# Optimization experiments

Hardware: AMD Instinct MI355X
Metric: run time of the kernel (lower is better)

The kernel has to match this reference:

```python
import jax, jax.numpy as jnp
import numpy as np

B, T, F_, S, H = 4096, 128, 96, 128, 512
IMPUTE_WEIGHT = 0.3
L1, L2 = 0.01, 0.1


def setup_inputs() -> dict:
    key = jax.random.key(0)
    ks = jax.random.split(key, 28)
    def n(k, shape, s=0.05):
        return jax.random.normal(k, shape, jnp.float32) * s
    return dict(
        values=jax.random.normal(ks[0], (B, T, F_), jnp.float32),
        masks=jax.random.bernoulli(ks[1], 0.8, (B, T, F_)).astype(jnp.float32),
        deltas=jax.random.uniform(ks[2], (B, T, F_), jnp.float32, 0.0, 5.0),
        statics=jax.random.normal(ks[3], (B, S), jnp.float32),
        static_masks=jax.random.bernoulli(ks[4], 0.8, (B, S)).astype(jnp.float32),
        labels=jax.random.bernoulli(ks[5], 0.5, (B,)).astype(jnp.float32),
        fr_W=n(ks[6], (S, S)), fr_b=n(ks[7], (S,)),
        d1_W=n(ks[8], (H, S)), d1_b=n(ks[9], (H,)),
        d2_W=n(ks[10], (H, H)), d2_b=n(ks[11], (H,)),
        d3_W=n(ks[12], (H, H)), d3_b=n(ks[13], (H,)),
        td_W=n(ks[14], (H, F_)), td_b=n(ks[15], (H,)),
        hist_W=n(ks[16], (F_, H)), hist_b=n(ks[17], (F_,)),
        st_W=n(ks[18], (F_, S)), st_b=n(ks[19], (F_,)),
        real_W=n(ks[20], (F_, F_)), real_b=n(ks[21], (F_,)),
        lstm_Wih=n(ks[22], (4 * H, 2 * F_)), lstm_Whh=n(ks[23], (4 * H, H)),
        lstm_bih=n(ks[24], (4 * H,)), lstm_bhh=n(ks[25], (4 * H,)),
        out_W=n(ks[26], (1, H)), out_b=n(ks[27], (1,)),
    )


def reference(values, masks, deltas, statics, static_masks, labels,
              fr_W, fr_b, d1_W, d1_b, d2_W, d2_b, d3_W, d3_b,
              td_W, td_b, hist_W, hist_b, st_W, st_b, real_W, real_b,
              lstm_Wih, lstm_Whh, lstm_bih, lstm_bhh, out_W, out_b):
    sg = jax.lax.stop_gradient
    # ---- MultiModal (dropout = identity in inference) ----
    s_h = statics @ fr_W.T + fr_b
    s_c = static_masks * statics + (1.0 - static_masks) * s_h
    s_tc = s_c
    s_loss = jnp.sum(jnp.abs(statics - s_c) * static_masks) / (jnp.sum(static_masks) + 1e-5)
    s_loss = s_loss + IMPUTE_WEIGHT * L2 * jnp.sum(jnp.abs(jnp.diagonal(sg(fr_W))))
    h = jax.nn.relu(s_c @ d1_W.T + d1_b)
    h = jax.nn.relu(h @ d2_W.T + d2_b)
    h = jax.nn.relu(h @ d3_W.T + d3_b)                 # initial hidden state
    c = jnp.zeros((values.shape[0], H), values.dtype)
    st_term = s_tc @ st_W.T + st_b

    def step(carry, xs):
        h, c, xl = carry
        x, m, d = xs                                   # each [B, F_]
        gamma = jnp.exp(-jax.nn.relu(d @ td_W.T + td_b))
        h = h * gamma
        x_c = (x @ real_W.T + real_b) + (h @ hist_W.T + hist_b) + st_term
        xl = xl + jnp.sum(jnp.abs(x - x_c) * m) / (jnp.sum(m) + 1e-5)
        c_c = m * x + (1.0 - m) * x_c
        inp = jnp.concatenate([c_c, m], axis=1)        # [B, 2*F_]
        gates = inp @ lstm_Wih.T + lstm_bih + h @ lstm_Whh.T + lstm_bhh
        i, f, g, o = jnp.split(gates, 4, axis=1)       # torch LSTMCell gate order
        c = jax.nn.sigmoid(f) * c + jax.nn.sigmoid(i) * jnp.tanh(g)
        h = jax.nn.sigmoid(o) * jnp.tanh(c)
        return (h, c, xl), c_c

    xs = (jnp.swapaxes(values, 0, 1), jnp.swapaxes(masks, 0, 1), jnp.swapaxes(deltas, 0, 1))
    (h, c, x_loss), imps = jax.lax.scan(step, (h, c, jnp.float32(0.0)), xs)
    imputations = jnp.swapaxes(imps, 0, 1)             # [B, T, F_]

    y_h = h @ out_W.T + out_b                          # [B, 1]
    z = y_h[:, 0]
    # BCE with logits, mean reduction (stable form)
    y_loss = jnp.mean(jnp.maximum(z, 0.0) - z * labels + jnp.log1p(jnp.exp(-jnp.abs(z))))
    # regularizers on .data (stop-gradient in torch semantics)
    r_loss = L1 * (jnp.sum(jnp.abs(sg(real_W))) + jnp.sum(jnp.abs(sg(hist_W))) + jnp.sum(jnp.abs(sg(st_W))))
    r_loss = r_loss + L2 * jnp.sum(jnp.abs(jnp.diagonal(sg(real_W))))
    loss = y_loss + r_loss + IMPUTE_WEIGHT * x_loss + s_loss
    return (loss, jax.nn.sigmoid(y_h), imputations)
```

## Files before the change

### kernel.cpp

```cpp
#include <hip/hip_runtime.h>
#include <math.h>

#define Bn 4096
#define Tn 128
#define Fn 96
#define Sn 128
#define Hn 512

typedef __attribute__((ext_vector_type(8))) short bf16x8;
typedef __attribute__((ext_vector_type(4))) float f32x4;

#define GC(p) ((const __attribute__((address_space(1))) void*)(p))
#define LC(p) ((__attribute__((address_space(3))) void*)(p))

__device__ __forceinline__ short tobf(float f){
  unsigned u = __float_as_uint(f);
  unsigned r = (u + 0x7fffu + ((u>>16)&1u)) >> 16;
  return (short)r;
}
__device__ __forceinline__ float bf2f(short s){
  return __uint_as_float(((unsigned)(unsigned short)s)<<16);
}
__device__ __forceinline__ float sigmf_(float x){ return 1.0f/(1.0f+expf(-x)); }

__device__ __forceinline__ int haddr(int row, int k){
  int c = k & 63;
  return ((k>>6)<<10) + (row<<6) + ((((c>>3) ^ (row&7)))<<3) + (c&7);
}

__device__ __forceinline__ void stage_tile(const short* gsrc, size_t sstride, int k0,
                                           short* lt, int rows, int wid, int lane, int nw){
  int calls = rows >> 3;
  for (int c = wid; c < calls; c += nw){
    int r = (c<<3) + (lane>>3);
    int ch = (lane&7) ^ (r&7);
    const short* gp = gsrc + (size_t)r*sstride + k0 + (ch<<3);
    __builtin_amdgcn_global_load_lds(GC(gp), LC(lt + (c<<9)), 16, 0, 0);
  }
}
__device__ __forceinline__ bf16x8 frag(const short* lt, int row, int ch){
  return *(const bf16x8*)(lt + (row<<6) + ((ch ^ (row&7))<<3));
}


__global__ void k_pack_td(const float* __restrict__ tdW, short* __restrict__ tdWp){
  int i = blockIdx.x*256 + threadIdx.x;
  if (i >= 512*128) return;
  int n = i>>7, k = i&127;
  tdWp[i] = (k < Fn) ? tobf(tdW[n*Fn + k]) : (short)0;
}
__global__ void k_pack_x(const float* __restrict__ realW, const float* __restrict__ histW,
                         const float* __restrict__ realb, const float* __restrict__ histb,
                         short* __restrict__ Wxp, float* __restrict__ bxp){
  int i = blockIdx.x*256 + threadIdx.x;
  if (i < Fn) bxp[i] = realb[i] + histb[i];
  if (i >= Fn*640) return;
  int f = i/640, k = i - f*640;
  float v = 0.f;
  if (k < 512) v = histW[f*Hn + k];
  else if (k < 608) v = realW[f*Fn + (k-512)];
  Wxp[i] = tobf(v);
}
__global__ void k_pack_g(const float* __restrict__ Wih, const float* __restrict__ Whh,
                         const float* __restrict__ bih, const float* __restrict__ bhh,
                         short* __restrict__ Wgp, float* __restrict__ bgp){
  int i = blockIdx.x*256 + threadIdx.x;
  if (i >= 16*128*704) return;
  int k = i % 704; int nc = i / 704;
  int pb = nc >> 7, ncol = nc & 127;
  int jj = pb*32 + (ncol >> 2), g = ncol & 3;
  int n = g*Hn + jj;
  float v;
  if (k < 512) v = Whh[(size_t)n*Hn + k];
  else if (k < 608) v = Wih[(size_t)n*192 + (k-512)];
  else v = Wih[(size_t)n*192 + 96 + (k-608)];
  Wgp[i] = tobf(v);
  if (k == 0) bgp[nc] = bih[n] + bhh[n];
}
__global__ void k_cvt(const float* __restrict__ src, short* __restrict__ dst, int n){
  int i = blockIdx.x*256 + threadIdx.x;
  if (i < n) dst[i] = tobf(src[i]);
}


__global__ void k_static(const float* __restrict__ statics, const float* __restrict__ smask,
                         const float* __restrict__ frW, const float* __restrict__ frb,
                         float* __restrict__ s_c){
  __shared__ float row[Sn];
  int b = blockIdx.x, j = threadIdx.x;
  row[j] = statics[b*Sn + j];
  __syncthreads();
  float acc = frb[j];
  #pragma unroll 4
  for (int k = 0; k < Sn; k++) acc += row[k] * frW[j*Sn + k];
  float m = smask[b*Sn + j];
  s_c[b*Sn + j] = m * row[j] + (1.0f - m) * acc;
}

template<int K, bool RELU, bool WF32>
__global__ __launch_bounds__(512) void k_gemm(const short* __restrict__ A,
    const short* __restrict__ B, const float* __restrict__ bias,
    short* __restrict__ outb, float* __restrict__ outf){
  __shared__ __align__(16) short stA[2][8192], stB[2][8192];
  const int tid = threadIdx.x, lane = tid&63, wid = tid>>6;
  const int mb = blockIdx.x >> 2, nb = blockIdx.x & 3;
  const int r0 = mb*128, c0 = nb*128;
  const int wM = wid>>1, wN = wid&1, lr = lane&15, lq = lane>>4;
  f32x4 acc[2][4];
  #pragma unroll
  for (int m=0;m<2;m++)
    #pragma unroll
    for (int n=0;n<4;n++) acc[m][n] = (f32x4){0,0,0,0};
  constexpr int NS = K/64;
  stage_tile(A + (size_t)r0*K, K, 0, stA[0], 128, wid, lane, 8);
  stage_tile(B + (size_t)c0*K, K, 0, stB[0], 128, wid, lane, 8);
  __syncthreads();
  for (int kc=0; kc<NS; kc++){
    if (kc < NS-1){
      stage_tile(A + (size_t)r0*K, K, (kc+1)*64, stA[(kc+1)&1], 128, wid, lane, 8);
      stage_tile(B + (size_t)c0*K, K, (kc+1)*64, stB[(kc+1)&1], 128, wid, lane, 8);
    }
    #pragma unroll
    for (int kk=0;kk<2;kk++){
      int ch = (kk<<2) + lq;
      bf16x8 af[2];
      #pragma unroll
      for (int m=0;m<2;m++) af[m] = frag(stA[kc&1], wM*32 + m*16 + lr, ch);
      #pragma unroll
      for (int n=0;n<4;n++){
        bf16x8 bf = frag(stB[kc&1], wN*64 + n*16 + lr, ch);
        #pragma unroll
        for (int m=0;m<2;m++)
          acc[m][n] = __builtin_amdgcn_mfma_f32_16x16x32_bf16(af[m], bf, acc[m][n],0,0,0);
      }
    }
    __syncthreads();
  }
  #pragma unroll
  for (int m=0;m<2;m++)
    #pragma unroll
    for (int n=0;n<4;n++){
      int col = c0 + wN*64 + n*16 + lr;
      float bv = bias[col];
      #pragma unroll
      for (int reg=0;reg<4;reg++){
        int row = r0 + wM*32 + m*16 + (lq<<2) + reg;
        float v = acc[m][n][reg] + bv;
        if (RELU) v = fmaxf(v, 0.f);
        outb[(size_t)row*512 + col] = tobf(v);
        if (WF32) outf[(size_t)row*512 + col] = v;
      }
    }
}

template<int K, int N, bool RELU>
__global__ void k_mlp(const float* __restrict__ in, const float* __restrict__ W,
                      const float* __restrict__ bias, float* __restrict__ out){
  __shared__ float row[K];
  int b = blockIdx.x;
  for (int i = threadIdx.x; i < K; i += blockDim.x) row[i] = in[b*K + i];
  __syncthreads();
  for (int n = threadIdx.x; n < N; n += blockDim.x){
    float acc = bias[n];
    #pragma unroll 4
    for (int k = 0; k < K; k++) acc += row[k] * W[n*K + k];
    if (RELU) acc = fmaxf(acc, 0.0f);
    out[b*N + n] = acc;
  }
}

__global__ __launch_bounds__(512) void k_dxc(int t,
    const float* __restrict__ values, const float* __restrict__ masks,
    const float* __restrict__ deltas,
    const short* __restrict__ tdWp, const float* __restrict__ tdb,
    const short* __restrict__ Wxp,  const float* __restrict__ bxp,
    const float* __restrict__ st,   const float* __restrict__ h_g,
    short* __restrict__ inp, float* __restrict__ out_imp,
    float* __restrict__ num, float* __restrict__ den){
  __shared__ __align__(16) short Adel[2*1024];
  __shared__ __align__(16) short A2[10*1024];
  __shared__ short sm[16*96];
  __shared__ __align__(16) short Bbig[65536];
  __shared__ float wred[8], wred2[8];
  const int tid = threadIdx.x, lane = tid&63, wid = tid>>6;
  const int r0 = blockIdx.x*16;
  const int lr = lane&15, lq = lane>>4;

  float4 xv4, mv4, dv4;
  const bool act = tid < 384;
  int ar=0, af0=0;
  if (act){
    ar = tid/24; int fq = tid - ar*24; af0 = fq*4;
    size_t gb = ((size_t)(r0+ar)*Tn + t)*Fn + af0;
    xv4 = *(const float4*)(values + gb);
    mv4 = *(const float4*)(masks  + gb);
    dv4 = *(const float4*)(deltas + gb);
  }

  float hreg[16];
  #pragma unroll
  for (int nq=0;nq<4;nq++){
    int col = nq*128 + wid*16 + lr;
    #pragma unroll
    for (int reg=0;reg<4;reg++)
      hreg[nq*4+reg] = h_g[(size_t)(r0 + (lq<<2) + reg)*Hn + col];
  }
  float streg[4] = {0.f,0.f,0.f,0.f};
  if (wid < 6){
    int f = wid*16 + lr;
    #pragma unroll
    for (int reg=0;reg<4;reg++)
      streg[reg] = st[(size_t)(r0 + (lq<<2) + reg)*Fn + f];
  }

  #pragma unroll
  for (int s=0; s<8; s++){
    int nq = s>>1, kc = s&1;
    stage_tile(tdWp + (size_t)(nq*128)*128, 128, kc*64, Bbig + s*8192, 128, wid, lane, 8);
  }

  if (act){
    #pragma unroll
    for (int j=0;j<4;j++){
      int f = af0 + j;
      float xv = ((const float*)&xv4)[j];
      float mv = ((const float*)&mv4)[j];
      float dv = ((const float*)&dv4)[j];
      sm[ar*96 + f] = tobf(mv);
      inp[(size_t)(r0+ar)*704 + 608 + f] = tobf(mv);
      A2 [haddr(ar, 512+f)] = tobf(xv);
      Adel[haddr(ar, f)]    = tobf(dv);
    }
  }
  { int r = tid>>5, cz = tid&31;
    Adel[haddr(r,  96+cz)] = 0;
    A2  [haddr(r, 608+cz)] = 0;
  }
  __syncthreads();

  f32x4 accd[4];
  #pragma unroll
  for (int q=0;q<4;q++) accd[q] = (f32x4){0,0,0,0};
  #pragma unroll
  for (int s=0; s<8; s++){
    int nq = s>>1, kc = s&1;
    #pragma unroll
    for (int kk=0;kk<2;kk++){
      int ch = (kk<<2) + lq;
      bf16x8 afr = frag(Adel + kc*1024, lr, ch);
      bf16x8 bfr = frag(Bbig + s*8192, wid*16 + lr, ch);
      accd[nq] = __builtin_amdgcn_mfma_f32_16x16x32_bf16(afr, bfr, accd[nq], 0,0,0);
    }
  }
  __syncthreads();

  #pragma unroll
  for (int kx=0; kx<10; kx++)
    stage_tile(Wxp, 640, kx*64, Bbig + kx*6144, 96, wid, lane, 8);

  #pragma unroll
  for (int nq=0;nq<4;nq++){
    int col = nq*128 + wid*16 + lr;
    float tb = tdb[col];
    #pragma unroll
    for (int reg=0;reg<4;reg++){
      int row = (lq<<2) + reg;
      float v = accd[nq][reg] + tb;
      float hd = hreg[nq*4+reg] * __expf(-fmaxf(v,0.f));
      A2[haddr(row, col)] = tobf(hd);
      inp[(size_t)(r0+row)*704 + col] = tobf(hd);
    }
  }
  __syncthreads();

  f32x4 accx = (f32x4){0,0,0,0};
  if (wid < 6){
    #pragma unroll
    for (int kx=0; kx<10; kx++)
      #pragma unroll
      for (int kk=0;kk<2;kk++){
        int ch = (kk<<2) + lq;
        bf16x8 afr = frag(A2 + kx*1024, lr, ch);
        bf16x8 bfr = frag(Bbig + kx*6144, wid*16 + lr, ch);
        accx = __builtin_amdgcn_mfma_f32_16x16x32_bf16(afr, bfr, accx, 0,0,0);
      }
  }
  float lsum = 0.f, msum = 0.f;
  if (wid < 6){
    int f = wid*16 + lr;
    float bx = bxp[f];
    #pragma unroll
    for (int reg=0;reg<4;reg++){
      int row = (lq<<2) + reg;
      float xcv = accx[reg] + bx + streg[reg];
      float xv = bf2f(A2[haddr(row, 512+f)]);
      float mv = bf2f(sm[row*96 + f]);
      lsum += fabsf(xv - xcv)*mv;
      msum += mv;
      float cc = mv*xv + (1.f-mv)*xcv;
      inp[(size_t)(r0+row)*704 + 512 + f] = tobf(cc);
      out_imp[((size_t)(r0+row)*Tn + t)*Fn + f] = cc;
    }
  }
  #pragma unroll
  for (int o=32;o>0;o>>=1){ lsum += __shfl_down(lsum, o); msum += __shfl_down(msum, o); }
  if (lane==0){ wred[wid] = lsum; wred2[wid] = msum; }
  __syncthreads();
  if (tid==0){
    float s2 = 0.f, s3 = 0.f;
    #pragma unroll
    for (int w2=0;w2<8;w2++){ s2 += wred[w2]; s3 += wred2[w2]; }
    atomicAdd(&num[t], s2);
    atomicAdd(&den[t], s3);
  }
}

__global__ __launch_bounds__(512, 4) void k_gates(int t, const short* __restrict__ inp,
    const short* __restrict__ Wgp, const float* __restrict__ bgp,
    float* __restrict__ h_g, float* __restrict__ c_g){
  __shared__ __align__(16) short stA[2][8192], stB[2][8192];
  const int tid = threadIdx.x, lane = tid&63, wid = tid>>6;
  const int mb = blockIdx.x & 31, pb = blockIdx.x >> 5;
  const int r0 = mb*128;
  const short* gA = inp + (size_t)r0*704;
  const short* gB = Wgp + (size_t)pb*128*704;
  const int wM = wid>>1, wN = wid&1, lr = lane&15, lq = lane>>4;
  f32x4 acc[2][4];
  #pragma unroll
  for (int m=0;m<2;m++)
    #pragma unroll
    for (int n=0;n<4;n++) acc[m][n] = (f32x4){0,0,0,0};

  stage_tile(gA, 704, 0, stA[0], 128, wid, lane, 8);
  stage_tile(gB, 704, 0, stB[0], 128, wid, lane, 8);
  __syncthreads();

  for (int kc=0; kc<11; kc++){
    if (kc < 10){
      stage_tile(gA, 704, (kc+1)*64, stA[(kc+1)&1], 128, wid, lane, 8);
      stage_tile(gB, 704, (kc+1)*64, stB[(kc+1)&1], 128, wid, lane, 8);
    }
    #pragma unroll
    for (int kk=0;kk<2;kk++){
      int ch = (kk<<2) + lq;
      bf16x8 af[2];
      #pragma unroll
      for (int m=0;m<2;m++) af[m] = frag(stA[kc&1], wM*32 + m*16 + lr, ch);
      #pragma unroll
      for (int n=0;n<4;n++){
        bf16x8 bf = frag(stB[kc&1], wN*64 + n*16 + lr, ch);
        #pragma unroll
        for (int m=0;m<2;m++)
          acc[m][n] = __builtin_amdgcn_mfma_f32_16x16x32_bf16(af[m], bf, acc[m][n],0,0,0);
      }
    }
    __syncthreads();
  }

  const int g = lane&3;
  const float s_  = (g==2) ? 2.0f : -1.0f;
  const float ca_ = (g==2) ? -2.0f : 1.0f;
  const float cb_ = (g==2) ? 1.0f : 0.0f;
  #pragma unroll
  for (int m=0;m<2;m++){
    int row = r0 + wM*32 + m*16 + (lq<<2) + g;
    #pragma unroll
    for (int n=0;n<4;n++){
      int colbase = wN*64 + n*16 + lr;
      float b = bgp[pb*128 + colbase];
      float q0 = 1.f/(1.f+__expf(s_*(acc[m][n][0]+b))); float a0 = q0*ca_+cb_;
      float q1 = 1.f/(1.f+__expf(s_*(acc[m][n][1]+b))); float a1 = q1*ca_+cb_;
      float q2 = 1.f/(1.f+__expf(s_*(acc[m][n][2]+b))); float a2 = q2*ca_+cb_;
      float q3 = 1.f/(1.f+__expf(s_*(acc[m][n][3]+b))); float a3 = q3*ca_+cb_;
      int i1=g^1, i2=g^2, i3=g^3;
      float p1 = (i1==0)?a0:(i1==1)?a1:(i1==2)?a2:a3;
      float p2 = (i2==0)?a0:(i2==1)?a1:(i2==2)?a2:a3;
      float p3 = (i3==0)?a0:(i3==1)?a1:(i3==2)?a2:a3;
      float ow = (g==0)?a0:(g==1)?a1:(g==2)?a2:a3;
      float t1 = __shfl_xor(p1, 1, 64);
      float t2 = __shfl_xor(p2, 2, 64);
      float t3 = __shfl_xor(p3, 3, 64);
      float si = (g==0)?ow:(g==1)?t1:(g==2)?t2:t3;
      float sf = (g==1)?ow:(g==0)?t1:(g==3)?t2:t3;
      float tg = (g==2)?ow:(g==3)?t1:(g==0)?t2:t3;
      float so = (g==3)?ow:(g==2)?t1:(g==1)?t2:t3;
      int jh = pb*32 + (colbase>>2);
      size_t idx = (size_t)row*Hn + jh;
      float co = c_g[idx];
      float cn = sf*co + si*tg;
      float targ = fminf(fmaxf(2.0f*cn,-60.f),60.f);
      float e = __expf(targ); float th = (e-1.f)/(e+1.f);
      c_g[idx] = cn;
      h_g[idx] = so*th;
    }
  }
}


__global__ void k_out(const float* __restrict__ h_g, const float* __restrict__ outW,
                      const float* __restrict__ outb, const float* __restrict__ labels,
                      float* __restrict__ out_sig, float* __restrict__ yacc){
  int b = blockIdx.x, lane = threadIdx.x;
  float s = 0.f;
  for (int k = lane; k < Hn; k += 64) s += h_g[(size_t)b*Hn + k] * outW[k];
  #pragma unroll
  for (int o = 32; o > 0; o >>= 1) s += __shfl_down(s, o);
  if (lane == 0){
    float z = s + outb[0];
    out_sig[b] = sigmf_(z);
    float yl = fmaxf(z, 0.f) - z*labels[b] + log1pf(expf(-fabsf(z)));
    atomicAdd(yacc, yl);
  }
}

__global__ void k_loss(const float* __restrict__ realW, const float* __restrict__ histW,
                       const float* __restrict__ stW,   const float* __restrict__ frW,
                       const float* __restrict__ num,   const float* __restrict__ den,
                       const float* __restrict__ yacc,  float* __restrict__ out0){
  int tid = threadIdx.x;
  float r1 = 0.f;
  for (int i = tid; i < Fn*Fn; i += 256) r1 += fabsf(realW[i]);
  for (int i = tid; i < Fn*Hn; i += 256) r1 += fabsf(histW[i]);
  for (int i = tid; i < Fn*Sn; i += 256) r1 += fabsf(stW[i]);
  float rd = 0.f;
  for (int i = tid; i < Fn; i += 256) rd += fabsf(realW[i*Fn + i]);
  float fd = 0.f;
  for (int i = tid; i < Sn; i += 256) fd += fabsf(frW[i*Sn + i]);
  float xl = 0.f;
  for (int t = tid; t < Tn; t += 256) xl += num[t] / (den[t] + 1e-5f);
  float v = 0.01f*r1 + 0.1f*rd + 0.3f*xl + 0.03f*fd;
  __shared__ float red[256];
  red[tid] = v; __syncthreads();
  for (int o = 128; o > 0; o >>= 1){ if (tid < o) red[tid] += red[tid + o]; __syncthreads(); }
  if (tid == 0) out0[0] = red[0] + yacc[0] / (float)Bn;
}


extern "C" void kernel_launch(void* const* d_in, const int* in_sizes, int n_in,
                              void* d_out, int out_size, void* d_ws, size_t ws_size,
                              hipStream_t stream){
  const float* values = (const float*)d_in[0];
  const float* masks  = (const float*)d_in[1];
  const float* deltas = (const float*)d_in[2];
  const float* statics= (const float*)d_in[3];
  const float* smask  = (const float*)d_in[4];
  const float* labels = (const float*)d_in[5];
  const float* frW = (const float*)d_in[6];
  const float* frb = (const float*)d_in[7];
  const float* d1W = (const float*)d_in[8];
  const float* d1b = (const float*)d_in[9];
  const float* d2W = (const float*)d_in[10];
  const float* d2b = (const float*)d_in[11];
  const float* d3W = (const float*)d_in[12];
  const float* d3b = (const float*)d_in[13];
  const float* tdW = (const float*)d_in[14];
  const float* tdb = (const float*)d_in[15];
  const float* histW = (const float*)d_in[16];
  const float* histb = (const float*)d_in[17];
  const float* stW = (const float*)d_in[18];
  const float* stb = (const float*)d_in[19];
  const float* realW = (const float*)d_in[20];
  const float* realb = (const float*)d_in[21];
  const float* Wih = (const float*)d_in[22];
  const float* Whh = (const float*)d_in[23];
  const float* bih = (const float*)d_in[24];
  const float* bhh = (const float*)d_in[25];
  const float* outW = (const float*)d_in[26];
  const float* outb = (const float*)d_in[27];

  float* out0    = (float*)d_out;
  float* out_sig = out0 + 1;
  float* out_imp = out0 + 1 + Bn;

  float* wsf  = (float*)d_ws;
  float* s_c  = wsf;  wsf += Bn*Sn;
  float* h    = wsf;  wsf += (size_t)Bn*Hn;
  float* c    = wsf;  wsf += (size_t)Bn*Hn;
  float* st   = wsf;  wsf += Bn*Fn;
  float* den  = wsf;  wsf += Tn;
  float* num  = wsf;  wsf += Tn;
  float* yacc = num + Tn;
  wsf += 1;
  float* bxp  = wsf;  wsf += 128;
  float* bgp  = wsf;  wsf += 2048;
  size_t off = ((size_t)(wsf - (float*)d_ws) + 3u) & ~(size_t)3u;
  short* wss  = (short*)((float*)d_ws + off);
  short* tdWp = wss;  wss += 512*128;
  short* Wxp  = wss;  wss += 96*640;
  short* Wgp  = wss;  wss += (size_t)16*128*704;
  short* inp  = wss;  wss += (size_t)Bn*704;
  short* wd1  = wss;  wss += 512*128;
  short* wd2  = wss;  wss += 512*512;
  short* wd3  = wss;  wss += 512*512;
  short* act0 = wss;  wss += (size_t)Bn*128;
  short* actA = wss;  wss += (size_t)Bn*512;
  short* actB = wss;  wss += (size_t)Bn*512;

  hipMemsetAsync(c,   0, (size_t)Bn*Hn*sizeof(float), stream);
  hipMemsetAsync(den, 0, (2*Tn + 1)*sizeof(float), stream);

  k_pack_td<<<(512*128+255)/256, 256, 0, stream>>>(tdW, tdWp);
  k_pack_x <<<(96*640+255)/256, 256, 0, stream>>>(realW, histW, realb, histb, Wxp, bxp);
  k_pack_g <<<(16*128*704+255)/256, 256, 0, stream>>>(Wih, Whh, bih, bhh, Wgp, bgp);
  k_cvt<<<(512*128+255)/256, 256, 0, stream>>>(d1W, wd1, 512*128);
  k_cvt<<<(512*512+255)/256, 256, 0, stream>>>(d2W, wd2, 512*512);
  k_cvt<<<(512*512+255)/256, 256, 0, stream>>>(d3W, wd3, 512*512);

  k_static<<<Bn, Sn, 0, stream>>>(statics, smask, frW, frb, s_c);
  k_cvt<<<(Bn*Sn+255)/256, 256, 0, stream>>>(s_c, act0, Bn*Sn);
  k_gemm<128, true,  false><<<128, 512, 0, stream>>>(act0, wd1, d1b, actA, (float*)nullptr);
  k_gemm<512, true,  false><<<128, 512, 0, stream>>>(actA, wd2, d2b, actB, (float*)nullptr);
  k_gemm<512, true,  true ><<<128, 512, 0, stream>>>(actB, wd3, d3b, actA, h);
  k_mlp<Sn, Fn, false><<<Bn, 256, 0, stream>>>(s_c, stW, stb, st);

  for (int t = 0; t < Tn; t++){
    k_dxc  <<<Bn/16,       512, 0, stream>>>(t, values, masks, deltas, tdWp, tdb,
                                             Wxp, bxp, st, h, inp, out_imp, num, den);
    k_gates<<<(Bn/128)*16, 512, 0, stream>>>(t, inp, Wgp, bgp, h, c);
  }

  k_out<<<Bn, 64, 0, stream>>>(h, outW, outb, labels, out_sig, yacc);
  k_loss<<<1, 256, 0, stream>>>(realW, histW, stW, frW, num, den, yacc, out0);
}
```

Before: 5.349 ms.

## Fuse next-step temporal decay GEMM into LSTM gates kernel epilogue

Moves the temporal-decay computation (deltas @ td_W, exp decay of h) for step t+1 into the epilogue of the k_gates kernel at step t, so the freshly computed hidden state is decayed while still in registers. A separate k_dec0 kernel handles step 0, and the input buffer is double-buffered so step t+1 can be written while step t is still read. The per-step x/c kernel becomes lighter and loads the decayed h from global memory instead of recomputing it. The goal is to drop the h_g reload and the decay GEMM from the serial dxc kernel; in exchange the gates kernel does extra work, a deltas load and extra syncs, which may affect its occupancy.

```diff
diff --git a/kernel.cpp b/kernel.cpp
--- a/kernel.cpp
+++ b/kernel.cpp
@@ -26,6 +26,10 @@
 __device__ __forceinline__ int haddr(int row, int k){
   int c = k & 63;
   return ((k>>6)<<10) + (row<<6) + ((((c>>3) ^ (row&7)))<<3) + (c&7);
+}
+__device__ __forceinline__ int haddr128(int row, int k){
+  int c = k & 63;
+  return ((k>>6)<<13) + (row<<6) + ((((c>>3) ^ (row&7)))<<3) + (c&7);
 }
 
 __device__ __forceinline__ void stage_tile(const short* gsrc, size_t sstride, int k0,
@@ -169,34 +173,23 @@
   }
 }
 
-__global__ __launch_bounds__(512) void k_dxc(int t,
-    const float* __restrict__ values, const float* __restrict__ masks,
-    const float* __restrict__ deltas,
-    const short* __restrict__ tdWp, const float* __restrict__ tdb,
-    const short* __restrict__ Wxp,  const float* __restrict__ bxp,
-    const float* __restrict__ st,   const float* __restrict__ h_g,
-    short* __restrict__ inp, float* __restrict__ out_imp,
-    float* __restrict__ num, float* __restrict__ den){
+__global__ __launch_bounds__(512) void k_dec0(
+    const float* __restrict__ deltas, const short* __restrict__ tdWp,
+    const float* __restrict__ tdb, const float* __restrict__ h_g,
+    short* __restrict__ inp){
   __shared__ __align__(16) short Adel[2*1024];
-  __shared__ __align__(16) short A2[10*1024];
-  __shared__ short sm[16*96];
   __shared__ __align__(16) short Bbig[65536];
-  __shared__ float wred[8], wred2[8];
   const int tid = threadIdx.x, lane = tid&63, wid = tid>>6;
   const int r0 = blockIdx.x*16;
   const int lr = lane&15, lq = lane>>4;
 
-  float4 xv4, mv4, dv4;
+  float4 dv4;
   const bool act = tid < 384;
   int ar=0, af0=0;
   if (act){
-    ar = tid/24; int fq = tid - ar*24; af0 = fq*4;
-    size_t gb = ((size_t)(r0+ar)*Tn + t)*Fn + af0;
-    xv4 = *(const float4*)(values + gb);
-    mv4 = *(const float4*)(masks  + gb);
-    dv4 = *(const float4*)(deltas + gb);
-  }
-
+    ar = tid/24; af0 = (tid - ar*24)*4;
+    dv4 = *(const float4*)(deltas + (size_t)(r0+ar)*Tn*Fn + af0);
+  }
   float hreg[16];
   #pragma unroll
   for (int nq=0;nq<4;nq++){
@@ -205,37 +198,15 @@
     for (int reg=0;reg<4;reg++)
       hreg[nq*4+reg] = h_g[(size_t)(r0 + (lq<<2) + reg)*Hn + col];
   }
-  float streg[4] = {0.f,0.f,0.f,0.f};
-  if (wid < 6){
-    int f = wid*16 + lr;
-    #pragma unroll
-    for (int reg=0;reg<4;reg++)
-      streg[reg] = st[(size_t)(r0 + (lq<<2) + reg)*Fn + f];
-  }
-
-  #pragma unroll
-  for (int s=0; s<8; s++){
-    int nq = s>>1, kc = s&1;
-    stage_tile(tdWp + (size_t)(nq*128)*128, 128, kc*64, Bbig + s*8192, 128, wid, lane, 8);
-  }
-
+  #pragma unroll
+  for (int s=0; s<8; s++)
+    stage_tile(tdWp + (size_t)((s>>1)*128)*128, 128, (s&1)*64, Bbig + s*8192, 128, wid, lane, 8);
   if (act){
     #pragma unroll
-    for (int j=0;j<4;j++){
-      int f = af0 + j;
-      float xv = ((const float*)&xv4)[j];
-      float mv = ((const float*)&mv4)[j];
-      float dv = ((const float*)&dv4)[j];
-      sm[ar*96 + f] = tobf(mv);
-      inp[(size_t)(r0+ar)*704 + 608 + f] = tobf(mv);
-      A2 [haddr(ar, 512+f)] = tobf(xv);
-      Adel[haddr(ar, f)]    = tobf(dv);
-    }
-  }
-  { int r = tid>>5, cz = tid&31;
-    Adel[haddr(r,  96+cz)] = 0;
-    A2  [haddr(r, 608+cz)] = 0;
-  }
+    for (int j=0;j<4;j++)
+      Adel[haddr(ar, af0+j)] = tobf(((const float*)&dv4)[j]);
+  }
+  { int r = tid>>5, cz = tid&31; Adel[haddr(r, 96+cz)] = 0; }
   __syncthreads();
 
   f32x4 accd[4];
@@ -252,12 +223,6 @@
       accd[nq] = __builtin_amdgcn_mfma_f32_16x16x32_bf16(afr, bfr, accd[nq], 0,0,0);
     }
   }
-  __syncthreads();
-
-  #pragma unroll
-  for (int kx=0; kx<10; kx++)
-    stage_tile(Wxp, 640, kx*64, Bbig + kx*6144, 96, wid, lane, 8);
-
   #pragma unroll
   for (int nq=0;nq<4;nq++){
     int col = nq*128 + wid*16 + lr;
@@ -266,11 +231,65 @@
     for (int reg=0;reg<4;reg++){
       int row = (lq<<2) + reg;
       float v = accd[nq][reg] + tb;
-      float hd = hreg[nq*4+reg] * __expf(-fmaxf(v,0.f));
-      A2[haddr(row, col)] = tobf(hd);
-      inp[(size_t)(r0+row)*704 + col] = tobf(hd);
-    }
-  }
+      inp[(size_t)(r0+row)*704 + col] = tobf(hreg[nq*4+reg] * __expf(-fmaxf(v,0.f)));
+    }
+  }
+}
+
+__global__ __launch_bounds__(512) void k_xc2(int t,
+    const float* __restrict__ values, const float* __restrict__ masks,
+    const short* __restrict__ Wxp,  const float* __restrict__ bxp,
+    const float* __restrict__ st,
+    short* __restrict__ inp, float* __restrict__ out_imp,
+    float* __restrict__ num, float* __restrict__ den){
+  __shared__ __align__(16) short A2[10*1024];
+  __shared__ short sm[16*96];
+  __shared__ __align__(16) short Bbig[61440];
+  __shared__ float wred[8], wred2[8];
+  const int tid = threadIdx.x, lane = tid&63, wid = tid>>6;
+  const int r0 = blockIdx.x*16;
+  const int lr = lane&15, lq = lane>>4;
+
+  float4 xv4, mv4;
+  const bool act = tid < 384;
+  int ar=0, af0=0;
+  if (act){
+    ar = tid/24; af0 = (tid - ar*24)*4;
+    size_t gb = ((size_t)(r0+ar)*Tn + t)*Fn + af0;
+    xv4 = *(const float4*)(values + gb);
+    mv4 = *(const float4*)(masks  + gb);
+  }
+  float streg[4] = {0.f,0.f,0.f,0.f};
+  if (wid < 6){
+    int f = wid*16 + lr;
+    #pragma unroll
+    for (int reg=0;reg<4;reg++)
+      streg[reg] = st[(size_t)(r0 + (lq<<2) + reg)*Fn + f];
+  }
+
+  for (int c2 = wid; c2 < 16; c2 += 8){
+    int chunk = c2 >> 1, rg = c2 & 1;
+    int r = rg*8 + (lane>>3);
+    int ch = (lane&7) ^ (r&7);
+    const short* gp = inp + (size_t)(r0 + r)*704 + chunk*64 + (ch<<3);
+    __builtin_amdgcn_global_load_lds(GC(gp), LC(A2 + chunk*1024 + rg*512), 16, 0, 0);
+  }
+  #pragma unroll
+  for (int kx=0; kx<10; kx++)
+    stage_tile(Wxp, 640, kx*64, Bbig + kx*6144, 96, wid, lane, 8);
+
+  if (act){
+    #pragma unroll
+    for (int j=0;j<4;j++){
+      int f = af0 + j;
+      float xv = ((const float*)&xv4)[j];
+      float mv = ((const float*)&mv4)[j];
+      sm[ar*96 + f] = tobf(mv);
+      inp[(size_t)(r0+ar)*704 + 608 + f] = tobf(mv);
+      A2[haddr(ar, 512+f)] = tobf(xv);
+    }
+  }
+  { int r = tid>>5, cz = tid&31; A2[haddr(r, 608+cz)] = 0; }
   __syncthreads();
 
   f32x4 accx = (f32x4){0,0,0,0};
@@ -315,40 +334,44 @@
   }
 }
 
-__global__ __launch_bounds__(512, 4) void k_gates(int t, const short* __restrict__ inp,
+__global__ __launch_bounds__(512, 4) void k_gates(int t,
+    const short* __restrict__ inpR, short* __restrict__ inpW,
     const short* __restrict__ Wgp, const float* __restrict__ bgp,
+    const float* __restrict__ deltas, const short* __restrict__ tdWp,
+    const float* __restrict__ tdb,
     float* __restrict__ h_g, float* __restrict__ c_g){
-  __shared__ __align__(16) short stA[2][8192], stB[2][8192];
+  __shared__ __align__(16) short SMEM[32768];
   const int tid = threadIdx.x, lane = tid&63, wid = tid>>6;
   const int mb = blockIdx.x & 31, pb = blockIdx.x >> 5;
   const int r0 = mb*128;
-  const short* gA = inp + (size_t)r0*704;
+  const short* gA = inpR + (size_t)r0*704;
   const short* gB = Wgp + (size_t)pb*128*704;
   const int wM = wid>>1, wN = wid&1, lr = lane&15, lq = lane>>4;
+  const bool hg = (t+1 < Tn);
   f32x4 acc[2][4];
   #pragma unroll
   for (int m=0;m<2;m++)
     #pragma unroll
     for (int n=0;n<4;n++) acc[m][n] = (f32x4){0,0,0,0};
 
-  stage_tile(gA, 704, 0, stA[0], 128, wid, lane, 8);
-  stage_tile(gB, 704, 0, stB[0], 128, wid, lane, 8);
+  stage_tile(gA, 704, 0, SMEM, 128, wid, lane, 8);
+  stage_tile(gB, 704, 0, SMEM + 16384, 128, wid, lane, 8);
   __syncthreads();
 
   for (int kc=0; kc<11; kc++){
     if (kc < 10){
-      stage_tile(gA, 704, (kc+1)*64, stA[(kc+1)&1], 128, wid, lane, 8);
-      stage_tile(gB, 704, (kc+1)*64, stB[(kc+1)&1], 128, wid, lane, 8);
+      stage_tile(gA, 704, (kc+1)*64, SMEM + ((kc+1)&1)*8192, 128, wid, lane, 8);
+      stage_tile(gB, 704, (kc+1)*64, SMEM + 16384 + ((kc+1)&1)*8192, 128, wid, lane, 8);
     }
     #pragma unroll
     for (int kk=0;kk<2;kk++){
       int ch = (kk<<2) + lq;
       bf16x8 af[2];
       #pragma unroll
-      for (int m=0;m<2;m++) af[m] = frag(stA[kc&1], wM*32 + m*16 + lr, ch);
+      for (int m=0;m<2;m++) af[m] = frag(SMEM + (kc&1)*8192, wM*32 + m*16 + lr, ch);
       #pragma unroll
       for (int n=0;n<4;n++){
-        bf16x8 bf = frag(stB[kc&1], wN*64 + n*16 + lr, ch);
+        bf16x8 bf = frag(SMEM + 16384 + (kc&1)*8192, wN*64 + n*16 + lr, ch);
         #pragma unroll
         for (int m=0;m<2;m++)
           acc[m][n] = __builtin_amdgcn_mfma_f32_16x16x32_bf16(af[m], bf, acc[m][n],0,0,0);
@@ -357,10 +380,24 @@
     __syncthreads();
   }
 
+  float dreg[24];
+  const int drow = tid>>2, dc0 = (tid&3)*24;
+  if (hg){
+    size_t gb = ((size_t)(r0+drow)*Tn + (t+1))*Fn + dc0;
+    #pragma unroll
+    for (int q=0;q<6;q++){
+      float4 v4 = *(const float4*)(deltas + gb + q*4);
+      dreg[q*4+0]=v4.x; dreg[q*4+1]=v4.y; dreg[q*4+2]=v4.z; dreg[q*4+3]=v4.w;
+    }
+    stage_tile(tdWp + (size_t)(pb*32)*128, 128, 0,  SMEM + 16384, 32, wid, lane, 8);
+    stage_tile(tdWp + (size_t)(pb*32)*128, 128, 64, SMEM + 18432, 32, wid, lane, 8);
+  }
+
   const int g = lane&3;
   const float s_  = (g==2) ? 2.0f : -1.0f;
   const float ca_ = (g==2) ? -2.0f : 1.0f;
   const float cb_ = (g==2) ? 1.0f : 0.0f;
+  float hnew[2][4];
   #pragma unroll
   for (int m=0;m<2;m++){
     int row = r0 + wM*32 + m*16 + (lq<<2) + g;
@@ -391,7 +428,56 @@
       float targ = fminf(fmaxf(2.0f*cn,-60.f),60.f);
       float e = __expf(targ); float th = (e-1.f)/(e+1.f);
       c_g[idx] = cn;
-      h_g[idx] = so*th;
+      float hv = so*th;
+      h_g[idx] = hv;
+      hnew[m][n] = hv;
+    }
+  }
+
+  if (hg){
+    #pragma unroll
+    for (int j=0;j<24;j++){
+      int cdx = dc0 + j;
+      SMEM[haddr128(drow, cdx)] = tobf(dreg[j]);
+    }
+    #pragma unroll
+    for (int j=0;j<8;j++){
+      int cdx = 96 + (tid&3)*8 + j;
+      SMEM[haddr128(drow, cdx)] = 0;
+    }
+    __syncthreads();
+
+    f32x4 gv[2];
+    gv[0]=(f32x4){0,0,0,0}; gv[1]=(f32x4){0,0,0,0};
+    #pragma unroll
+    for (int kc=0;kc<2;kc++)
+      #pragma unroll
+      for (int kk=0;kk<2;kk++){
+        int ch = (kk<<2) + lq;
+        bf16x8 afr = frag(SMEM + kc*8192, wid*16 + lr, ch);
+        #pragma unroll
+        for (int n=0;n<2;n++)
+          gv[n] = __builtin_amdgcn_mfma_f32_16x16x32_bf16(afr,
+                    frag(SMEM + 16384 + kc*2048, n*16 + lr, ch), gv[n], 0,0,0);
+      }
+    float* vlds = (float*)(SMEM + 20480);
+    #pragma unroll
+    for (int n=0;n<2;n++)
+      #pragma unroll
+      for (int reg=0;reg<4;reg++)
+        vlds[(wid*16 + (lq<<2) + reg)*33 + n*16 + lr] = gv[n][reg];
+    __syncthreads();
+
+    #pragma unroll
+    for (int m=0;m<2;m++){
+      int rowl = wM*32 + m*16 + (lq<<2) + g;
+      #pragma unroll
+      for (int n=0;n<4;n++){
+        int jl = (wN*64 + n*16 + lr)>>2;
+        float v = vlds[rowl*33 + jl] + tdb[pb*32 + jl];
+        float gam = __expf(-fmaxf(v, 0.f));
+        inpW[(size_t)(r0+rowl)*704 + pb*32 + jl] = tobf(hnew[m][n] * gam);
+      }
     }
   }
 }
@@ -488,7 +574,8 @@
   short* tdWp = wss;  wss += 512*128;
   short* Wxp  = wss;  wss += 96*640;
   short* Wgp  = wss;  wss += (size_t)16*128*704;
-  short* inp  = wss;  wss += (size_t)Bn*704;
+  short* inp0 = wss;  wss += (size_t)Bn*704;
+  short* inp1 = wss;  wss += (size_t)Bn*704;
   short* wd1  = wss;  wss += 512*128;
   short* wd2  = wss;  wss += 512*512;
   short* wd3  = wss;  wss += 512*512;
@@ -513,10 +600,15 @@
   k_gemm<512, true,  true ><<<128, 512, 0, stream>>>(actB, wd3, d3b, actA, h);
   k_mlp<Sn, Fn, false><<<Bn, 256, 0, stream>>>(s_c, stW, stb, st);
 
+  k_dec0<<<Bn/16, 512, 0, stream>>>(deltas, tdWp, tdb, h, inp0);
+
   for (int t = 0; t < Tn; t++){
-    k_dxc  <<<Bn/16,       512, 0, stream>>>(t, values, masks, deltas, tdWp, tdb,
-                                             Wxp, bxp, st, h, inp, out_imp, num, den);
-    k_gates<<<(Bn/128)*16, 512, 0, stream>>>(t, inp, Wgp, bgp, h, c);
+    short* iR = (t & 1) ? inp1 : inp0;
+    short* iW = (t & 1) ? inp0 : inp1;
+    k_xc2  <<<Bn/16,       512, 0, stream>>>(t, values, masks, Wxp, bxp, st,
+                                             iR, out_imp, num, den);
+    k_gates<<<(Bn/128)*16, 512, 0, stream>>>(t, iR, iW, Wgp, bgp,
+                                             deltas, tdWp, tdb, h, c);
   }
 
   k_out<<<Bn, 64, 0, stream>>>(h, outW, outb, labels, out_sig, yacc);
```

New measurement: 5.327 ms. No clear change (-0.4%).
